# Kernel optimization log

Measured on AMD Instinct MI355X. Metric: run time of the kernel, lower is better.

Reference implementation:

```python
import jax, jax.numpy as jnp
import numpy as np


def setup_inputs() -> dict:
    key = jax.random.key(0)
    k1, k2 = jax.random.split(key)
    B, H, W, C, S = 128, 32, 32, 64, 64
    x = jax.random.normal(k1, (B, H, W, C), dtype=jnp.float32)
    # accumulators are positive linear-space weights (log is taken in forward)
    accumulators = jax.random.uniform(k2, (H, W, C, S), dtype=jnp.float32, minval=1e-4, maxval=1.0)
    return {"x": x, "accumulators": accumulators}


def reference(x, accumulators):
    # x: [B, H, W, C]; accumulators: [H, W, C, S] (positive, linear space)
    log_w = jnp.log(accumulators)
    # normalize weights over the input-channel axis (axis=2), per scope & sum
    log_w = jax.nn.log_softmax(log_w, axis=2)  # [H, W, C, S]
    # stable per-scope log-domain matmul: log(exp(x) @ exp(log_w))
    mx = jnp.max(x, axis=-1, keepdims=True)        # [B, H, W, 1]
    mw = jnp.max(log_w, axis=2)                    # [H, W, S]
    prod = jnp.einsum("bhwc,hwcs->bhws", jnp.exp(x - mx), jnp.exp(log_w - mw[:, :, None, :]))
    out = jnp.log(prod) + mx + mw                  # [B, H, W, S]
    return out
```

## Files before the change

kernel.cpp:

```cpp
#include <hip/hip_runtime.h>


typedef __attribute__((ext_vector_type(8))) short s8v;
typedef __attribute__((ext_vector_type(4))) float f4v;

__device__ __forceinline__ unsigned short f2bf(float f) {
    unsigned int u = __float_as_uint(f);
    u += 0x7FFFu + ((u >> 16) & 1u);
    return (unsigned short)(u >> 16);
}

__global__ __launch_bounds__(256) void sls_kernel(
    const float* __restrict__ x,
    const float* __restrict__ acc,
    float* __restrict__ out)
{
    const int hw   = blockIdx.x;
    const int t    = threadIdx.x;
    const int lane = t & 63;
    const int quad = lane >> 4;
    const int nn   = lane & 15;
    const int wave = t >> 6;

    __shared__ unsigned short e_lds[2][64 * 72];

    const int r0 = t >> 4;
    const int c0 = (t & 15) * 4;
    const float* xbase = x + (size_t)hw * 64 + c0;

    f4v xv0[4], xv1[4];
    #pragma unroll
    for (int it = 0; it < 4; ++it)
        xv0[it] = *(const f4v*)(xbase + (size_t)(r0 + 16 * it) * 65536);

    const int ni = wave;
    const float* accb = acc + (size_t)hw * 4096 + ni * 16 + nn;
    float bv[2][8];
    #pragma unroll
    for (int ks = 0; ks < 2; ++ks)
        #pragma unroll
        for (int j = 0; j < 8; ++j)
            bv[ks][j] = accb[(ks * 32 + quad * 8 + j) * 64];

    #pragma unroll
    for (int it = 0; it < 4; ++it)
        xv1[it] = *(const f4v*)(xbase + (size_t)(64 + r0 + 16 * it) * 65536);

    #pragma unroll
    for (int it = 0; it < 4; ++it) {
        f4v v = xv0[it];
        const int row = r0 + 16 * it;
        ushort4 pk;
        pk.x = f2bf(__expf(v.x));
        pk.y = f2bf(__expf(v.y));
        pk.z = f2bf(__expf(v.z));
        pk.w = f2bf(__expf(v.w));
        *(ushort4*)&e_lds[0][row * 72 + c0] = pk;
    }

    float csum = 0.f;
    #pragma unroll
    for (int ks = 0; ks < 2; ++ks)
        #pragma unroll
        for (int j = 0; j < 8; ++j) csum += bv[ks][j];
    csum += __shfl_xor(csum, 16);
    csum += __shfl_xor(csum, 32);
    const float lsum_n = __logf(csum);

    s8v bf0, bf1;
    #pragma unroll
    for (int j = 0; j < 8; ++j) {
        bf0[j] = (short)f2bf(bv[0][j]);
        bf1[j] = (short)f2bf(bv[1][j]);
    }

    __syncthreads();

    float* outp = out + (size_t)hw * 64 + ni * 16 + nn;
    #pragma unroll
    for (int mi = 0; mi < 4; ++mi) {
        const unsigned short* rowp = &e_lds[0][(mi * 16 + nn) * 72];
        s8v a0 = *(const s8v*)(rowp + quad * 8);
        s8v a1 = *(const s8v*)(rowp + 32 + quad * 8);
        f4v d = {0.f, 0.f, 0.f, 0.f};
        d = __builtin_amdgcn_mfma_f32_16x16x32_bf16(a0, bf0, d, 0, 0, 0);
        d = __builtin_amdgcn_mfma_f32_16x16x32_bf16(a1, bf1, d, 0, 0, 0);
        #pragma unroll
        for (int r = 0; r < 4; ++r) {
            const int b_row = mi * 16 + quad * 4 + r;
            __builtin_nontemporal_store(__logf(d[r]) - lsum_n, outp + (size_t)b_row * 65536);
        }
    }

    #pragma unroll
    for (int it = 0; it < 4; ++it) {
        f4v v = xv1[it];
        const int row = r0 + 16 * it;
        ushort4 pk;
        pk.x = f2bf(__expf(v.x));
        pk.y = f2bf(__expf(v.y));
        pk.z = f2bf(__expf(v.z));
        pk.w = f2bf(__expf(v.w));
        *(ushort4*)&e_lds[1][row * 72 + c0] = pk;
    }
    __syncthreads();

    #pragma unroll
    for (int mi = 0; mi < 4; ++mi) {
        const unsigned short* rowp = &e_lds[1][(mi * 16 + nn) * 72];
        s8v a0 = *(const s8v*)(rowp + quad * 8);
        s8v a1 = *(const s8v*)(rowp + 32 + quad * 8);
        f4v d = {0.f, 0.f, 0.f, 0.f};
        d = __builtin_amdgcn_mfma_f32_16x16x32_bf16(a0, bf0, d, 0, 0, 0);
        d = __builtin_amdgcn_mfma_f32_16x16x32_bf16(a1, bf1, d, 0, 0, 0);
        #pragma unroll
        for (int r = 0; r < 4; ++r) {
            const int b_row = 64 + mi * 16 + quad * 4 + r;
            __builtin_nontemporal_store(__logf(d[r]) - lsum_n, outp + (size_t)b_row * 65536);
        }
    }
}

extern "C" void kernel_launch(void* const* d_in, const int* in_sizes, int n_in,
                              void* d_out, int out_size, void* d_ws, size_t ws_size,
                              hipStream_t stream) {
    const float* x   = (const float*)d_in[0];
    const float* acc = (const float*)d_in[1];
    float* out = (float*)d_out;
    (void)in_sizes; (void)n_in; (void)d_ws; (void)ws_size; (void)out_size;
    sls_kernel<<<dim3(1024), dim3(256), 0, stream>>>(x, acc, out);
}
```

Measured before the change: 96.71 us.

## Split batch across two blocks per scope to double grid parallelism

Each block now handles 64 batch rows for one (h,w) scope instead of 128, and the grid doubles to 2048 blocks. The in-block two-stage pipeline and the double-buffered LDS go away, and launch bounds request 8 blocks per CU. This is meant to raise occupancy and memory-level parallelism across the GPU. In exchange, the accumulator slice is loaded and its column sums recomputed twice per scope, and loads no longer overlap with compute inside a block.

Result: slower. 100.6 us (+4.1%).

```diff
diff --git a/kernel.cpp b/kernel.cpp
--- a/kernel.cpp
+++ b/kernel.cpp
@@ -10,31 +10,24 @@
     return (unsigned short)(u >> 16);
 }
 
-__global__ __launch_bounds__(256) void sls_kernel(
+__global__ __launch_bounds__(256, 8) void sls_kernel(
     const float* __restrict__ x,
     const float* __restrict__ acc,
     float* __restrict__ out)
 {
-    const int hw   = blockIdx.x;
+    const int hw   = blockIdx.x & 1023;
+    const int bb   = (blockIdx.x >> 10) << 6;
     const int t    = threadIdx.x;
-    const int lane = t & 63;
-    const int quad = lane >> 4;
-    const int nn   = lane & 15;
+    const int quad = (t >> 4) & 3;
+    const int nn   = t & 15;
     const int wave = t >> 6;
 
-    __shared__ unsigned short e_lds[2][64 * 72];
+    __shared__ unsigned short e_lds[64 * 72];
 
     const int r0 = t >> 4;
     const int c0 = (t & 15) * 4;
-    const float* xbase = x + (size_t)hw * 64 + c0;
 
-    f4v xv0[4], xv1[4];
-    #pragma unroll
-    for (int it = 0; it < 4; ++it)
-        xv0[it] = *(const f4v*)(xbase + (size_t)(r0 + 16 * it) * 65536);
-
-    const int ni = wave;
-    const float* accb = acc + (size_t)hw * 4096 + ni * 16 + nn;
+    const float* accb = acc + (size_t)hw * 4096 + wave * 16 + nn;
     float bv[2][8];
     #pragma unroll
     for (int ks = 0; ks < 2; ++ks)
@@ -42,20 +35,21 @@
         for (int j = 0; j < 8; ++j)
             bv[ks][j] = accb[(ks * 32 + quad * 8 + j) * 64];
 
+    const float* xbase = x + (size_t)(bb + r0) * 65536 + (size_t)hw * 64 + c0;
+    f4v xv[4];
     #pragma unroll
     for (int it = 0; it < 4; ++it)
-        xv1[it] = *(const f4v*)(xbase + (size_t)(64 + r0 + 16 * it) * 65536);
+        xv[it] = *(const f4v*)(xbase + (size_t)(16 * it) * 65536);
 
     #pragma unroll
     for (int it = 0; it < 4; ++it) {
-        f4v v = xv0[it];
-        const int row = r0 + 16 * it;
+        f4v v = xv[it];
         ushort4 pk;
         pk.x = f2bf(__expf(v.x));
         pk.y = f2bf(__expf(v.y));
         pk.z = f2bf(__expf(v.z));
         pk.w = f2bf(__expf(v.w));
-        *(ushort4*)&e_lds[0][row * 72 + c0] = pk;
+        *(ushort4*)&e_lds[(r0 + 16 * it) * 72 + c0] = pk;
     }
 
     float csum = 0.f;
@@ -76,10 +70,10 @@
 
     __syncthreads();
 
-    float* outp = out + (size_t)hw * 64 + ni * 16 + nn;
+    float* outp = out + (size_t)bb * 65536 + (size_t)hw * 64 + wave * 16 + nn;
     #pragma unroll
     for (int mi = 0; mi < 4; ++mi) {
-        const unsigned short* rowp = &e_lds[0][(mi * 16 + nn) * 72];
+        const unsigned short* rowp = &e_lds[(mi * 16 + nn) * 72];
         s8v a0 = *(const s8v*)(rowp + quad * 8);
         s8v a1 = *(const s8v*)(rowp + 32 + quad * 8);
         f4v d = {0.f, 0.f, 0.f, 0.f};
@@ -88,34 +82,6 @@
         #pragma unroll
         for (int r = 0; r < 4; ++r) {
             const int b_row = mi * 16 + quad * 4 + r;
-            __builtin_nontemporal_store(__logf(d[r]) - lsum_n, outp + (size_t)b_row * 65536);
-        }
-    }
-
-    #pragma unroll
-    for (int it = 0; it < 4; ++it) {
-        f4v v = xv1[it];
-        const int row = r0 + 16 * it;
-        ushort4 pk;
-        pk.x = f2bf(__expf(v.x));
-        pk.y = f2bf(__expf(v.y));
-        pk.z = f2bf(__expf(v.z));
-        pk.w = f2bf(__expf(v.w));
-        *(ushort4*)&e_lds[1][row * 72 + c0] = pk;
-    }
-    __syncthreads();
-
-    #pragma unroll
-    for (int mi = 0; mi < 4; ++mi) {
-        const unsigned short* rowp = &e_lds[1][(mi * 16 + nn) * 72];
-        s8v a0 = *(const s8v*)(rowp + quad * 8);
-        s8v a1 = *(const s8v*)(rowp + 32 + quad * 8);
-        f4v d = {0.f, 0.f, 0.f, 0.f};
-        d = __builtin_amdgcn_mfma_f32_16x16x32_bf16(a0, bf0, d, 0, 0, 0);
-        d = __builtin_amdgcn_mfma_f32_16x16x32_bf16(a1, bf1, d, 0, 0, 0);
-        #pragma unroll
-        for (int r = 0; r < 4; ++r) {
-            const int b_row = 64 + mi * 16 + quad * 4 + r;
             __builtin_nontemporal_store(__logf(d[r]) - lsum_n, outp + (size_t)b_row * 65536);
         }
     }
@@ -128,5 +94,5 @@
     const float* acc = (const float*)d_in[1];
     float* out = (float*)d_out;
     (void)in_sizes; (void)n_in; (void)d_ws; (void)ws_size; (void)out_size;
-    sls_kernel<<<dim3(1024), dim3(256), 0, stream>>>(x, acc, out);
+    sls_kernel<<<dim3(2048), dim3(256), 0, stream>>>(x, acc, out);
 }
```
